# Kernel optimization log

Hardware: AMD Instinct MI355X
Metric: run time of the kernel (lower is better)

Reference implementation:

```python
import jax, jax.numpy as jnp
import numpy as np


def setup_inputs() -> dict:
    key = jax.random.key(0)
    k1, k2, k3 = jax.random.split(key, 3)
    B, S_TOT, HD = 2, 4096, 1024
    return {
        "q": jax.random.normal(k1, (B, S_TOT, HD), dtype=jnp.float32),
        "k": jax.random.normal(k2, (B, S_TOT, HD), dtype=jnp.float32),
        "v": jax.random.normal(k3, (B, S_TOT, HD), dtype=jnp.float32),
        "num_heads": 16,
        "num_shots": 4,
        "per_g": 64,
    }


def reference(q, k, v, num_heads, num_shots, per_g):
    # Equal-length shots: shot_latent_indices = [0, L, 2L, ..., s_tot] per batch.
    b, s_tot, hd = q.shape
    d = hd // num_heads
    L = s_tot // num_shots  # local shot length
    scale = 1.0 / jnp.sqrt(jnp.asarray(d, q.dtype))

    # [b, S, L, H, D]
    qs = q.reshape(b, num_shots, L, num_heads, d)
    ks = k.reshape(b, num_shots, L, num_heads, d)
    vs = v.reshape(b, num_shots, L, num_heads, d)

    # Global pool: first per_g tokens of each shot ('firstk'), shared by all shots.
    kg = ks[:, :, :per_g].reshape(b, num_shots * per_g, num_heads, d)  # [b, G, H, D]
    vg = vs[:, :, :per_g].reshape(b, num_shots * per_g, num_heads, d)

    # Block-local scores [b,S,H,L,L] and shared-global scores [b,S,H,L,G]
    s_loc = jnp.einsum("bsqhd,bskhd->bshqk", qs, ks) * scale
    s_glb = jnp.einsum("bsqhd,bghd->bshqg", qs, kg) * scale
    logits = jnp.concatenate([s_loc, s_glb], axis=-1)  # [b,S,H,L,L+G]
    p = jax.nn.softmax(logits, axis=-1)

    o_loc = jnp.einsum("bshqk,bskhd->bsqhd", p[..., :L], vs)
    o_glb = jnp.einsum("bshqg,bghd->bsqhd", p[..., L:], vg)
    out = (o_loc + o_glb).reshape(b, s_tot, hd)
    return out
```

## Files before the change

### kernel.cpp

```cpp
#include <hip/hip_runtime.h>
#include <hip/hip_bf16.h>

#define S_TOT 4096
#define HDIM  1024
#define NH    16
#define DH    64
#define L_    1024
#define NT    19

using bf16x8 = __attribute__((ext_vector_type(8))) short;
using f32x16 = __attribute__((ext_vector_type(16))) float;
using i32x4  = __attribute__((ext_vector_type(4))) int;

typedef const __attribute__((address_space(1))) unsigned int* gp1_t;
typedef __attribute__((address_space(3))) unsigned int* lp3_t;

__device__ __forceinline__ short f2bf(float f) {
    union { float f; unsigned u; } x; x.f = f;
    unsigned r = x.u + 0x7FFFu + ((x.u >> 16) & 1u);
    return (short)(r >> 16);
}

__device__ __forceinline__ unsigned cvt_pk_bf16(float lo, float hi) {
    unsigned r;
    asm("v_cvt_pk_bf16_f32 %0, %1, %2" : "=v"(r) : "v"(lo), "v"(hi));
    return r;
}

__device__ __forceinline__ float exp2_fast(float x) {
#if __has_builtin(__builtin_amdgcn_exp2f)
    return __builtin_amdgcn_exp2f(x);
#else
    return exp2f(x);
#endif
}

__device__ __forceinline__ void gload16(const void* g, void* l) {
    __builtin_amdgcn_global_load_lds((gp1_t)g, (lp3_t)(unsigned long)(l), 16, 0, 0);
}

__global__ __launch_bounds__(256) void prep_kv(
    const float* __restrict__ kf, const float* __restrict__ vf,
    short* __restrict__ kb, short* __restrict__ vb)
{
    __shared__ short st[64 * 70];
    const int bid = blockIdx.x, tid = threadIdx.x;
    if (bid < 1024) {
        const int gid = bid * 256 + tid;
        #pragma unroll
        for (int it = 0; it < 2; ++it) {
            size_t e = ((size_t)gid + (size_t)it * 262144) * 16;
            #pragma unroll
            for (int half = 0; half < 2; ++half) {
                float4 a = *(const float4*)(kf + e + half * 8);
                float4 c = *(const float4*)(kf + e + half * 8 + 4);
                bf16x8 r;
                r[0]=f2bf(a.x); r[1]=f2bf(a.y); r[2]=f2bf(a.z); r[3]=f2bf(a.w);
                r[4]=f2bf(c.x); r[5]=f2bf(c.y); r[6]=f2bf(c.z); r[7]=f2bf(c.w);
                *(bf16x8*)(kb + e + half * 8) = r;
            }
        }
    } else {
        const int vbid = bid - 1024;
        const int stile = vbid & 63, ht = (vbid >> 6) & 15, b = vbid >> 10;
        const int rt = tid >> 2, q4 = tid & 3;
        const float* src = vf + ((size_t)(b * S_TOT + stile * 64 + rt)) * HDIM + ht * 64 + q4 * 16;
        short* dst = st + rt * 70 + q4 * 16;
        #pragma unroll
        for (int i = 0; i < 4; ++i) {
            float4 x = *(const float4*)(src + i * 4);
            dst[i*4+0] = f2bf(x.x); dst[i*4+1] = f2bf(x.y);
            dst[i*4+2] = f2bf(x.z); dst[i*4+3] = f2bf(x.w);
        }
        __syncthreads();
        const int orow = tid >> 2, oq = tid & 3;
        bf16x8 o0, o1;
        #pragma unroll
        for (int j = 0; j < 8; ++j) o0[j] = st[(oq * 16 + j) * 70 + orow];
        #pragma unroll
        for (int j = 0; j < 8; ++j) o1[j] = st[(oq * 16 + 8 + j) * 70 + orow];
        short* dst2 = vb + ((size_t)((b * NH + ht) * 64 + orow)) * S_TOT + stile * 64 + oq * 16;
        *(bf16x8*)dst2 = o0;
        *(bf16x8*)(dst2 + 8) = o1;
    }
}

__global__ __launch_bounds__(256, 2) void attn_kernel(
    const float* __restrict__ qf, const short* __restrict__ kb,
    const short* __restrict__ vb, float* __restrict__ out)
{
    __shared__ __align__(16) char smem[32768];
    const int tid  = threadIdx.x;
    const int wave = tid >> 6, lane = tid & 63;
    const int hi   = lane >> 5, q32 = lane & 31;

    const int bidhw = blockIdx.x;
    const int bid = ((bidhw & 7) << 6) | (bidhw >> 3);
    const int qt = bid & 3, h = (bid >> 2) & 15, s = (bid >> 6) & 3, b = bid >> 8;

    const float CSC = 0.125f * 1.4426950408889634f;
    bf16x8 qv[2][4];
    #pragma unroll
    for (int qs = 0; qs < 2; ++qs) {
        const float* qp = qf + ((size_t)(b*S_TOT + s*L_ + qt*256 + wave*64 + qs*32 + q32)) * HDIM
                             + h * DH + hi * 8;
        #pragma unroll
        for (int d = 0; d < 4; ++d) {
            float4 x0 = *(const float4*)(qp + d * 16);
            float4 x1 = *(const float4*)(qp + d * 16 + 4);
            i32x4 u;
            u[0] = (int)cvt_pk_bf16(x0.x * CSC, x0.y * CSC);
            u[1] = (int)cvt_pk_bf16(x0.z * CSC, x0.w * CSC);
            u[2] = (int)cvt_pk_bf16(x1.x * CSC, x1.y * CSC);
            u[3] = (int)cvt_pk_bf16(x1.z * CSC, x1.w * CSC);
            qv[qs][d] = __builtin_bit_cast(bf16x8, u);
        }
    }

    const int cid = tid, row = cid >> 3;
    const int lch = (cid & 7) ^ (row & 7);
    const int krow = (row & 0x33) | ((row & 4) << 1) | ((row & 8) >> 1);
    const size_t ko = (size_t)krow * 2048 + (lch << 4);
    const size_t vo = (size_t)row  * 8192 + (lch << 4);
    const char* kbase = (const char*)kb + ((size_t)b * S_TOT) * 2048 + h * 128;
    const char* vbase = (const char*)vb + ((size_t)(b * NH + h)) * (64ull * 8192);

    auto abs_tile_of = [&](int t) -> int {
        if (t < 16) return s * 16 + t;
        int g = t - 16; if (g >= s) ++g;
        return g * 16;
    };
    auto stage = [&](int t, int bo) {
        const int at = abs_tile_of(t);
        const char* kp = kbase + (size_t)at * 131072;
        const char* vp = vbase + (size_t)at * 128;
        char* dst = smem + bo + wave * 1024;
        gload16(kp + ko,          dst);
        gload16(kp + ko + 65536,  dst + 4096);
        gload16(vp + vo,          dst + 8192);
        gload16(vp + vo + 262144, dst + 12288);
    };

    int qc[4];
    #pragma unroll
    for (int i = 0; i < 4; ++i)
        qc[i] = q32 * 128 + (((i * 2 + hi) ^ (q32 & 7)) << 4);

    f32x16 zro;
    #pragma unroll
    for (int r = 0; r < 16; ++r) zro[r] = 0.f;
    f32x16 acc[2][2];
    acc[0][0] = zro; acc[0][1] = zro; acc[1][0] = zro; acc[1][1] = zro;
    float ps[2] = {0.f, 0.f};

    stage(0, 0);
    int bufo = 0;
    for (int t = 0; t < NT; ++t) {
        if (t + 1 < NT) {
            stage(t + 1, bufo ^ 16384);
            asm volatile("s_waitcnt vmcnt(4)" ::: "memory");
        } else {
            asm volatile("s_waitcnt vmcnt(0)" ::: "memory");
        }
        __builtin_amdgcn_sched_barrier(0);
        __builtin_amdgcn_s_barrier();
        __builtin_amdgcn_sched_barrier(0);
        const char* sb = smem + bufo;

        #pragma unroll
        for (int half = 0; half < 2; ++half) {
            const int koff = half * 4096;
            f32x16 S[2];
            __builtin_amdgcn_s_setprio(1);
            bf16x8 f0 = *(const bf16x8*)(sb + koff + qc[0]);
            bf16x8 f1 = *(const bf16x8*)(sb + koff + qc[1]);
            bf16x8 f2 = *(const bf16x8*)(sb + koff + qc[2]);
            bf16x8 f3 = *(const bf16x8*)(sb + koff + qc[3]);
            #pragma unroll
            for (int qs = 0; qs < 2; ++qs) {
                f32x16 a = __builtin_amdgcn_mfma_f32_32x32x16_bf16(f0, qv[qs][0], zro, 0,0,0);
                a = __builtin_amdgcn_mfma_f32_32x32x16_bf16(f1, qv[qs][1], a, 0,0,0);
                a = __builtin_amdgcn_mfma_f32_32x32x16_bf16(f2, qv[qs][2], a, 0,0,0);
                a = __builtin_amdgcn_mfma_f32_32x32x16_bf16(f3, qv[qs][3], a, 0,0,0);
                S[qs] = a;
            }
            __builtin_amdgcn_s_setprio(0);

            if (t == 0) {
                #pragma unroll
                for (int qs = 0; qs < 2; ++qs)
                    #pragma unroll
                    for (int r = 0; r < 16; ++r)
                        S[qs][r] = exp2_fast(S[qs][r] + 1.0f);
            } else {
                #pragma unroll
                for (int qs = 0; qs < 2; ++qs)
                    #pragma unroll
                    for (int r = 0; r < 16; ++r)
                        S[qs][r] = exp2_fast(S[qs][r]);
            }
            #pragma unroll
            for (int qs = 0; qs < 2; ++qs) {
                float s0 = (S[qs][0] + S[qs][1]) + (S[qs][2] + S[qs][3]);
                float s1 = (S[qs][4] + S[qs][5]) + (S[qs][6] + S[qs][7]);
                float s2 = (S[qs][8] + S[qs][9]) + (S[qs][10] + S[qs][11]);
                float s3 = (S[qs][12] + S[qs][13]) + (S[qs][14] + S[qs][15]);
                ps[qs] += (s0 + s1) + (s2 + s3);
            }

            bf16x8 pf[2][2];
            #pragma unroll
            for (int qs = 0; qs < 2; ++qs) {
                i32x4 u;
                u[0] = (int)cvt_pk_bf16(S[qs][0],  S[qs][1]);
                u[1] = (int)cvt_pk_bf16(S[qs][2],  S[qs][3]);
                u[2] = (int)cvt_pk_bf16(S[qs][4],  S[qs][5]);
                u[3] = (int)cvt_pk_bf16(S[qs][6],  S[qs][7]);
                pf[qs][0] = __builtin_bit_cast(bf16x8, u);
                u[0] = (int)cvt_pk_bf16(S[qs][8],  S[qs][9]);
                u[1] = (int)cvt_pk_bf16(S[qs][10], S[qs][11]);
                u[2] = (int)cvt_pk_bf16(S[qs][12], S[qs][13]);
                u[3] = (int)cvt_pk_bf16(S[qs][14], S[qs][15]);
                pf[qs][1] = __builtin_bit_cast(bf16x8, u);
            }

            __builtin_amdgcn_s_setprio(1);
            bf16x8 w00 = *(const bf16x8*)(sb + 8192  + qc[2*half]);
            bf16x8 w01 = *(const bf16x8*)(sb + 8192  + qc[2*half+1]);
            bf16x8 w10 = *(const bf16x8*)(sb + 12288 + qc[2*half]);
            bf16x8 w11 = *(const bf16x8*)(sb + 12288 + qc[2*half+1]);
            #pragma unroll
            for (int qs = 0; qs < 2; ++qs) {
                acc[qs][0] = __builtin_amdgcn_mfma_f32_32x32x16_bf16(w00, pf[qs][0], acc[qs][0], 0,0,0);
                acc[qs][0] = __builtin_amdgcn_mfma_f32_32x32x16_bf16(w01, pf[qs][1], acc[qs][0], 0,0,0);
                acc[qs][1] = __builtin_amdgcn_mfma_f32_32x32x16_bf16(w10, pf[qs][0], acc[qs][1], 0,0,0);
                acc[qs][1] = __builtin_amdgcn_mfma_f32_32x32x16_bf16(w11, pf[qs][1], acc[qs][1], 0,0,0);
            }
            __builtin_amdgcn_s_setprio(0);
        }

        __builtin_amdgcn_sched_barrier(0);
        __builtin_amdgcn_s_barrier();
        __builtin_amdgcn_sched_barrier(0);
        bufo ^= 16384;
    }

    #pragma unroll
    for (int qs = 0; qs < 2; ++qs) {
        float tot = ps[qs] + __shfl_xor(ps[qs], 32);
        float inv = 1.0f / tot;
        const size_t orow = (size_t)(b*S_TOT + s*L_ + qt*256 + wave*64 + qs*32 + q32);
        float* op = out + orow * HDIM + h * DH;
        #pragma unroll
        for (int m = 0; m < 4; ++m) {
            float4 w0, w1;
            w0.x = acc[qs][0][4*m+0]*inv; w0.y = acc[qs][0][4*m+1]*inv;
            w0.z = acc[qs][0][4*m+2]*inv; w0.w = acc[qs][0][4*m+3]*inv;
            *(float4*)(op + 8*m + 4*hi) = w0;
            w1.x = acc[qs][1][4*m+0]*inv; w1.y = acc[qs][1][4*m+1]*inv;
            w1.z = acc[qs][1][4*m+2]*inv; w1.w = acc[qs][1][4*m+3]*inv;
            *(float4*)(op + 32 + 8*m + 4*hi) = w1;
        }
    }
}

extern "C" void kernel_launch(void* const* d_in, const int* in_sizes, int n_in,
                              void* d_out, int out_size, void* d_ws, size_t ws_size,
                              hipStream_t stream) {
    const float* q = (const float*)d_in[0];
    const float* k = (const float*)d_in[1];
    const float* v = (const float*)d_in[2];
    char* ws = (char*)d_ws;
    short* kbuf = (short*)(ws);
    short* vbuf = (short*)(ws + (16u << 20));
    prep_kv<<<dim3(3072), dim3(256), 0, stream>>>(k, v, kbuf, vbuf);
    attn_kernel<<<dim3(512), dim3(256), 0, stream>>>(q, kbuf, vbuf, (float*)d_out);
}
```

Baseline: 71.22 us.

## Deepen K/V prefetch to two-tile stages with quad LDS buffering

Doubles shared memory to 64KB so that two K/V tiles are loaded per stage and two stages are in flight. Each barrier pair now covers two tiles, which halves the number of barriers per tile and hides more global-load latency behind the MFMA work. In exchange, LDS per block doubles, which could limit blocks per CU. The prologue also adds a full vmcnt(0) drain, and the last stage loads tile 18 twice because of index clamping.

```diff
diff --git a/kernel.cpp b/kernel.cpp
--- a/kernel.cpp
+++ b/kernel.cpp
@@ -89,7 +89,7 @@
     const float* __restrict__ qf, const short* __restrict__ kb,
     const short* __restrict__ vb, float* __restrict__ out)
 {
-    __shared__ __align__(16) char smem[32768];
+    __shared__ __align__(16) char smem[65536];
     const int tid  = threadIdx.x;
     const int wave = tid >> 6, lane = tid & 63;
     const int hi   = lane >> 5, q32 = lane & 31;
@@ -130,11 +130,11 @@
         int g = t - 16; if (g >= s) ++g;
         return g * 16;
     };
-    auto stage = [&](int t, int bo) {
+    auto stage = [&](int t, int rbase) {
         const int at = abs_tile_of(t);
         const char* kp = kbase + (size_t)at * 131072;
         const char* vp = vbase + (size_t)at * 128;
-        char* dst = smem + bo + wave * 1024;
+        char* dst = smem + rbase + wave * 1024;
         gload16(kp + ko,          dst);
         gload16(kp + ko + 65536,  dst + 4096);
         gload16(vp + vo,          dst + 8192);
@@ -153,97 +153,105 @@
     acc[0][0] = zro; acc[0][1] = zro; acc[1][0] = zro; acc[1][1] = zro;
     float ps[2] = {0.f, 0.f};
 
+    #define CHUNK(RB, HF, W2) do {                                                 \
+        f32x16 S_[2];                                                              \
+        {                                                                          \
+            __builtin_amdgcn_s_setprio(1);                                         \
+            bf16x8 f0 = *(const bf16x8*)(smem + (RB) + (HF)*4096 + qc[0]);         \
+            bf16x8 f1 = *(const bf16x8*)(smem + (RB) + (HF)*4096 + qc[1]);         \
+            bf16x8 f2 = *(const bf16x8*)(smem + (RB) + (HF)*4096 + qc[2]);         \
+            bf16x8 f3 = *(const bf16x8*)(smem + (RB) + (HF)*4096 + qc[3]);         \
+            _Pragma("unroll")                                                      \
+            for (int qs = 0; qs < 2; ++qs) {                                       \
+                f32x16 a = __builtin_amdgcn_mfma_f32_32x32x16_bf16(f0, qv[qs][0], zro, 0,0,0); \
+                a = __builtin_amdgcn_mfma_f32_32x32x16_bf16(f1, qv[qs][1], a, 0,0,0); \
+                a = __builtin_amdgcn_mfma_f32_32x32x16_bf16(f2, qv[qs][2], a, 0,0,0); \
+                a = __builtin_amdgcn_mfma_f32_32x32x16_bf16(f3, qv[qs][3], a, 0,0,0); \
+                S_[qs] = a;                                                        \
+            }                                                                      \
+            __builtin_amdgcn_s_setprio(0);                                         \
+        }                                                                          \
+        _Pragma("unroll")                                                          \
+        for (int qs = 0; qs < 2; ++qs) {                                           \
+            _Pragma("unroll")                                                      \
+            for (int r = 0; r < 16; ++r)                                           \
+                S_[qs][r] = (W2) ? exp2_fast(S_[qs][r] + 1.0f)                     \
+                                 : exp2_fast(S_[qs][r]);                           \
+            float s0 = (S_[qs][0] + S_[qs][1]) + (S_[qs][2] + S_[qs][3]);          \
+            float s1 = (S_[qs][4] + S_[qs][5]) + (S_[qs][6] + S_[qs][7]);          \
+            float s2 = (S_[qs][8] + S_[qs][9]) + (S_[qs][10] + S_[qs][11]);        \
+            float s3 = (S_[qs][12] + S_[qs][13]) + (S_[qs][14] + S_[qs][15]);      \
+            ps[qs] += (s0 + s1) + (s2 + s3);                                       \
+        }                                                                          \
+        bf16x8 pf0_[2], pf1_[2];                                                   \
+        _Pragma("unroll")                                                          \
+        for (int qs = 0; qs < 2; ++qs) {                                           \
+            i32x4 u;                                                               \
+            u[0] = (int)cvt_pk_bf16(S_[qs][0],  S_[qs][1]);                        \
+            u[1] = (int)cvt_pk_bf16(S_[qs][2],  S_[qs][3]);                        \
+            u[2] = (int)cvt_pk_bf16(S_[qs][4],  S_[qs][5]);                        \
+            u[3] = (int)cvt_pk_bf16(S_[qs][6],  S_[qs][7]);                        \
+            pf0_[qs] = __builtin_bit_cast(bf16x8, u);                              \
+            u[0] = (int)cvt_pk_bf16(S_[qs][8],  S_[qs][9]);                        \
+            u[1] = (int)cvt_pk_bf16(S_[qs][10], S_[qs][11]);                       \
+            u[2] = (int)cvt_pk_bf16(S_[qs][12], S_[qs][13]);                       \
+            u[3] = (int)cvt_pk_bf16(S_[qs][14], S_[qs][15]);                       \
+            pf1_[qs] = __builtin_bit_cast(bf16x8, u);                              \
+        }                                                                          \
+        {                                                                          \
+            __builtin_amdgcn_s_setprio(1);                                         \
+            bf16x8 w00 = *(const bf16x8*)(smem + (RB) + 8192  + qc[2*(HF)]);       \
+            bf16x8 w01 = *(const bf16x8*)(smem + (RB) + 8192  + qc[2*(HF)+1]);     \
+            bf16x8 w10 = *(const bf16x8*)(smem + (RB) + 12288 + qc[2*(HF)]);       \
+            bf16x8 w11 = *(const bf16x8*)(smem + (RB) + 12288 + qc[2*(HF)+1]);     \
+            _Pragma("unroll")                                                      \
+            for (int qs = 0; qs < 2; ++qs) {                                       \
+                acc[qs][0] = __builtin_amdgcn_mfma_f32_32x32x16_bf16(w00, pf0_[qs], acc[qs][0], 0,0,0); \
+                acc[qs][0] = __builtin_amdgcn_mfma_f32_32x32x16_bf16(w01, pf1_[qs], acc[qs][0], 0,0,0); \
+                acc[qs][1] = __builtin_amdgcn_mfma_f32_32x32x16_bf16(w10, pf0_[qs], acc[qs][1], 0,0,0); \
+                acc[qs][1] = __builtin_amdgcn_mfma_f32_32x32x16_bf16(w11, pf1_[qs], acc[qs][1], 0,0,0); \
+            }                                                                      \
+            __builtin_amdgcn_s_setprio(0);                                         \
+        }                                                                          \
+    } while (0)
+
+    #define BARRIER() do {                                                         \
+        __builtin_amdgcn_sched_barrier(0);                                         \
+        __builtin_amdgcn_s_barrier();                                              \
+        __builtin_amdgcn_sched_barrier(0);                                         \
+    } while (0)
+
     stage(0, 0);
-    int bufo = 0;
-    for (int t = 0; t < NT; ++t) {
-        if (t + 1 < NT) {
-            stage(t + 1, bufo ^ 16384);
-            asm volatile("s_waitcnt vmcnt(4)" ::: "memory");
-        } else {
-            asm volatile("s_waitcnt vmcnt(0)" ::: "memory");
-        }
-        __builtin_amdgcn_sched_barrier(0);
-        __builtin_amdgcn_s_barrier();
-        __builtin_amdgcn_sched_barrier(0);
-        const char* sb = smem + bufo;
-
-        #pragma unroll
-        for (int half = 0; half < 2; ++half) {
-            const int koff = half * 4096;
-            f32x16 S[2];
-            __builtin_amdgcn_s_setprio(1);
-            bf16x8 f0 = *(const bf16x8*)(sb + koff + qc[0]);
-            bf16x8 f1 = *(const bf16x8*)(sb + koff + qc[1]);
-            bf16x8 f2 = *(const bf16x8*)(sb + koff + qc[2]);
-            bf16x8 f3 = *(const bf16x8*)(sb + koff + qc[3]);
-            #pragma unroll
-            for (int qs = 0; qs < 2; ++qs) {
-                f32x16 a = __builtin_amdgcn_mfma_f32_32x32x16_bf16(f0, qv[qs][0], zro, 0,0,0);
-                a = __builtin_amdgcn_mfma_f32_32x32x16_bf16(f1, qv[qs][1], a, 0,0,0);
-                a = __builtin_amdgcn_mfma_f32_32x32x16_bf16(f2, qv[qs][2], a, 0,0,0);
-                a = __builtin_amdgcn_mfma_f32_32x32x16_bf16(f3, qv[qs][3], a, 0,0,0);
-                S[qs] = a;
-            }
-            __builtin_amdgcn_s_setprio(0);
-
-            if (t == 0) {
-                #pragma unroll
-                for (int qs = 0; qs < 2; ++qs)
-                    #pragma unroll
-                    for (int r = 0; r < 16; ++r)
-                        S[qs][r] = exp2_fast(S[qs][r] + 1.0f);
-            } else {
-                #pragma unroll
-                for (int qs = 0; qs < 2; ++qs)
-                    #pragma unroll
-                    for (int r = 0; r < 16; ++r)
-                        S[qs][r] = exp2_fast(S[qs][r]);
-            }
-            #pragma unroll
-            for (int qs = 0; qs < 2; ++qs) {
-                float s0 = (S[qs][0] + S[qs][1]) + (S[qs][2] + S[qs][3]);
-                float s1 = (S[qs][4] + S[qs][5]) + (S[qs][6] + S[qs][7]);
-                float s2 = (S[qs][8] + S[qs][9]) + (S[qs][10] + S[qs][11]);
-                float s3 = (S[qs][12] + S[qs][13]) + (S[qs][14] + S[qs][15]);
-                ps[qs] += (s0 + s1) + (s2 + s3);
-            }
-
-            bf16x8 pf[2][2];
-            #pragma unroll
-            for (int qs = 0; qs < 2; ++qs) {
-                i32x4 u;
-                u[0] = (int)cvt_pk_bf16(S[qs][0],  S[qs][1]);
-                u[1] = (int)cvt_pk_bf16(S[qs][2],  S[qs][3]);
-                u[2] = (int)cvt_pk_bf16(S[qs][4],  S[qs][5]);
-                u[3] = (int)cvt_pk_bf16(S[qs][6],  S[qs][7]);
-                pf[qs][0] = __builtin_bit_cast(bf16x8, u);
-                u[0] = (int)cvt_pk_bf16(S[qs][8],  S[qs][9]);
-                u[1] = (int)cvt_pk_bf16(S[qs][10], S[qs][11]);
-                u[2] = (int)cvt_pk_bf16(S[qs][12], S[qs][13]);
-                u[3] = (int)cvt_pk_bf16(S[qs][14], S[qs][15]);
-                pf[qs][1] = __builtin_bit_cast(bf16x8, u);
-            }
-
-            __builtin_amdgcn_s_setprio(1);
-            bf16x8 w00 = *(const bf16x8*)(sb + 8192  + qc[2*half]);
-            bf16x8 w01 = *(const bf16x8*)(sb + 8192  + qc[2*half+1]);
-            bf16x8 w10 = *(const bf16x8*)(sb + 12288 + qc[2*half]);
-            bf16x8 w11 = *(const bf16x8*)(sb + 12288 + qc[2*half+1]);
-            #pragma unroll
-            for (int qs = 0; qs < 2; ++qs) {
-                acc[qs][0] = __builtin_amdgcn_mfma_f32_32x32x16_bf16(w00, pf[qs][0], acc[qs][0], 0,0,0);
-                acc[qs][0] = __builtin_amdgcn_mfma_f32_32x32x16_bf16(w01, pf[qs][1], acc[qs][0], 0,0,0);
-                acc[qs][1] = __builtin_amdgcn_mfma_f32_32x32x16_bf16(w10, pf[qs][0], acc[qs][1], 0,0,0);
-                acc[qs][1] = __builtin_amdgcn_mfma_f32_32x32x16_bf16(w11, pf[qs][1], acc[qs][1], 0,0,0);
-            }
-            __builtin_amdgcn_s_setprio(0);
-        }
-
-        __builtin_amdgcn_sched_barrier(0);
-        __builtin_amdgcn_s_barrier();
-        __builtin_amdgcn_sched_barrier(0);
-        bufo ^= 16384;
-    }
+    stage(1, 16384);
+    asm volatile("s_waitcnt vmcnt(0)" ::: "memory");
+    BARRIER();
+
+    stage(2, 32768);
+    stage(3, 49152);
+    asm volatile("s_waitcnt vmcnt(8)" ::: "memory");
+    BARRIER();
+    CHUNK(0, 0, 1); CHUNK(0, 1, 1);
+    CHUNK(16384, 0, 0); CHUNK(16384, 1, 0);
+    BARRIER();
+
+    for (int j = 1; j < 9; ++j) {
+        const int rS = (j & 1) ? 0 : 32768;
+        const int rC = (j & 1) ? 32768 : 0;
+        int ts0 = 2*j + 2, ts1 = 2*j + 3;
+        if (ts0 > 18) ts0 = 18;
+        if (ts1 > 18) ts1 = 18;
+        stage(ts0, rS);
+        stage(ts1, rS + 16384);
+        asm volatile("s_waitcnt vmcnt(8)" ::: "memory");
+        BARRIER();
+        CHUNK(rC, 0, 0); CHUNK(rC, 1, 0);
+        CHUNK(rC + 16384, 0, 0); CHUNK(rC + 16384, 1, 0);
+        BARRIER();
+    }
+
+    asm volatile("s_waitcnt vmcnt(0)" ::: "memory");
+    BARRIER();
+    CHUNK(32768, 0, 0); CHUNK(32768, 1, 0);
 
     #pragma unroll
     for (int qs = 0; qs < 2; ++qs) {
```

Measured after the change: 75.27 us. 5.7% more time.

## Use 8 waves with one query block each and triple-buffered K/V staging

Applied to the files above, without the earlier changes.

Blocks grow from 256 to 512 threads, and each wave now owns 32 query rows instead of 64, which halves accumulator registers per wave. Staging moves from double to triple buffering in 48KB of LDS, prefetching two tiles ahead with a single barrier per iteration. The single-tile-half loop is replaced by interleaved score MFMAs over the full 64-key tile. The aim is more waves in flight and deeper latency hiding. The cost is more LDS per block, which may limit occupancy, and each K/V fragment read from LDS is reused by fewer MFMAs.

```diff
diff --git a/kernel.cpp b/kernel.cpp
--- a/kernel.cpp
+++ b/kernel.cpp
@@ -85,11 +85,11 @@
     }
 }
 
-__global__ __launch_bounds__(256, 2) void attn_kernel(
+__global__ __launch_bounds__(512, 2) void attn_kernel(
     const float* __restrict__ qf, const short* __restrict__ kb,
     const short* __restrict__ vb, float* __restrict__ out)
 {
-    __shared__ __align__(16) char smem[32768];
+    __shared__ __align__(16) char smem[49152];
     const int tid  = threadIdx.x;
     const int wave = tid >> 6, lane = tid & 63;
     const int hi   = lane >> 5, q32 = lane & 31;
@@ -99,25 +99,23 @@
     const int qt = bid & 3, h = (bid >> 2) & 15, s = (bid >> 6) & 3, b = bid >> 8;
 
     const float CSC = 0.125f * 1.4426950408889634f;
-    bf16x8 qv[2][4];
-    #pragma unroll
-    for (int qs = 0; qs < 2; ++qs) {
-        const float* qp = qf + ((size_t)(b*S_TOT + s*L_ + qt*256 + wave*64 + qs*32 + q32)) * HDIM
-                             + h * DH + hi * 8;
-        #pragma unroll
-        for (int d = 0; d < 4; ++d) {
-            float4 x0 = *(const float4*)(qp + d * 16);
-            float4 x1 = *(const float4*)(qp + d * 16 + 4);
-            i32x4 u;
-            u[0] = (int)cvt_pk_bf16(x0.x * CSC, x0.y * CSC);
-            u[1] = (int)cvt_pk_bf16(x0.z * CSC, x0.w * CSC);
-            u[2] = (int)cvt_pk_bf16(x1.x * CSC, x1.y * CSC);
-            u[3] = (int)cvt_pk_bf16(x1.z * CSC, x1.w * CSC);
-            qv[qs][d] = __builtin_bit_cast(bf16x8, u);
-        }
-    }
-
-    const int cid = tid, row = cid >> 3;
+    const float* qp = qf + ((size_t)(b*S_TOT + s*L_ + qt*256 + wave*32 + q32)) * HDIM
+                         + h * DH + hi * 8;
+    bf16x8 qv[4];
+    #pragma unroll
+    for (int d = 0; d < 4; ++d) {
+        float4 x0 = *(const float4*)(qp + d * 16);
+        float4 x1 = *(const float4*)(qp + d * 16 + 4);
+        i32x4 u;
+        u[0] = (int)cvt_pk_bf16(x0.x * CSC, x0.y * CSC);
+        u[1] = (int)cvt_pk_bf16(x0.z * CSC, x0.w * CSC);
+        u[2] = (int)cvt_pk_bf16(x1.x * CSC, x1.y * CSC);
+        u[3] = (int)cvt_pk_bf16(x1.z * CSC, x1.w * CSC);
+        qv[d] = __builtin_bit_cast(bf16x8, u);
+    }
+
+    const int cid = wave * 64 + lane;
+    const int row = cid >> 3;
     const int lch = (cid & 7) ^ (row & 7);
     const int krow = (row & 0x33) | ((row & 4) << 1) | ((row & 8) >> 1);
     const size_t ko = (size_t)krow * 2048 + (lch << 4);
@@ -134,11 +132,9 @@
         const int at = abs_tile_of(t);
         const char* kp = kbase + (size_t)at * 131072;
         const char* vp = vbase + (size_t)at * 128;
-        char* dst = smem + bo + wave * 1024;
-        gload16(kp + ko,          dst);
-        gload16(kp + ko + 65536,  dst + 4096);
-        gload16(vp + vo,          dst + 8192);
-        gload16(vp + vo + 262144, dst + 12288);
+        char* dK = smem + bo + wave * 1024;
+        gload16(kp + ko, dK);
+        gload16(vp + vo, dK + 8192);
     };
 
     int qc[4];
@@ -149,118 +145,109 @@
     f32x16 zro;
     #pragma unroll
     for (int r = 0; r < 16; ++r) zro[r] = 0.f;
-    f32x16 acc[2][2];
-    acc[0][0] = zro; acc[0][1] = zro; acc[1][0] = zro; acc[1][1] = zro;
-    float ps[2] = {0.f, 0.f};
+    f32x16 acc0 = zro, acc1 = zro;
+    float ps = 0.f;
 
     stage(0, 0);
-    int bufo = 0;
+    stage(1, 16384);
+    asm volatile("s_waitcnt vmcnt(0)" ::: "memory");
+
+    int rd = 0, nx = 16384, st = 32768;
     for (int t = 0; t < NT; ++t) {
-        if (t + 1 < NT) {
-            stage(t + 1, bufo ^ 16384);
-            asm volatile("s_waitcnt vmcnt(4)" ::: "memory");
-        } else {
-            asm volatile("s_waitcnt vmcnt(0)" ::: "memory");
-        }
         __builtin_amdgcn_sched_barrier(0);
         __builtin_amdgcn_s_barrier();
         __builtin_amdgcn_sched_barrier(0);
-        const char* sb = smem + bufo;
-
-        #pragma unroll
-        for (int half = 0; half < 2; ++half) {
-            const int koff = half * 4096;
-            f32x16 S[2];
+
+        if (t + 2 < NT) stage(t + 2, st);
+
+        const float bias = (t == 0) ? 1.0f : 0.0f;
+        const char* sb = smem + rd;
+
+        f32x16 sA, sB;
+        {
             __builtin_amdgcn_s_setprio(1);
-            bf16x8 f0 = *(const bf16x8*)(sb + koff + qc[0]);
-            bf16x8 f1 = *(const bf16x8*)(sb + koff + qc[1]);
-            bf16x8 f2 = *(const bf16x8*)(sb + koff + qc[2]);
-            bf16x8 f3 = *(const bf16x8*)(sb + koff + qc[3]);
-            #pragma unroll
-            for (int qs = 0; qs < 2; ++qs) {
-                f32x16 a = __builtin_amdgcn_mfma_f32_32x32x16_bf16(f0, qv[qs][0], zro, 0,0,0);
-                a = __builtin_amdgcn_mfma_f32_32x32x16_bf16(f1, qv[qs][1], a, 0,0,0);
-                a = __builtin_amdgcn_mfma_f32_32x32x16_bf16(f2, qv[qs][2], a, 0,0,0);
-                a = __builtin_amdgcn_mfma_f32_32x32x16_bf16(f3, qv[qs][3], a, 0,0,0);
-                S[qs] = a;
-            }
+            bf16x8 a0 = *(const bf16x8*)(sb + qc[0]);
+            bf16x8 b0 = *(const bf16x8*)(sb + 4096 + qc[0]);
+            sA = __builtin_amdgcn_mfma_f32_32x32x16_bf16(a0, qv[0], zro, 0,0,0);
+            sB = __builtin_amdgcn_mfma_f32_32x32x16_bf16(b0, qv[0], zro, 0,0,0);
+            bf16x8 a1 = *(const bf16x8*)(sb + qc[1]);
+            bf16x8 b1 = *(const bf16x8*)(sb + 4096 + qc[1]);
+            sA = __builtin_amdgcn_mfma_f32_32x32x16_bf16(a1, qv[1], sA, 0,0,0);
+            sB = __builtin_amdgcn_mfma_f32_32x32x16_bf16(b1, qv[1], sB, 0,0,0);
+            bf16x8 a2 = *(const bf16x8*)(sb + qc[2]);
+            bf16x8 b2 = *(const bf16x8*)(sb + 4096 + qc[2]);
+            sA = __builtin_amdgcn_mfma_f32_32x32x16_bf16(a2, qv[2], sA, 0,0,0);
+            sB = __builtin_amdgcn_mfma_f32_32x32x16_bf16(b2, qv[2], sB, 0,0,0);
+            bf16x8 a3 = *(const bf16x8*)(sb + qc[3]);
+            bf16x8 b3 = *(const bf16x8*)(sb + 4096 + qc[3]);
+            sA = __builtin_amdgcn_mfma_f32_32x32x16_bf16(a3, qv[3], sA, 0,0,0);
+            sB = __builtin_amdgcn_mfma_f32_32x32x16_bf16(b3, qv[3], sB, 0,0,0);
             __builtin_amdgcn_s_setprio(0);
-
-            if (t == 0) {
-                #pragma unroll
-                for (int qs = 0; qs < 2; ++qs)
-                    #pragma unroll
-                    for (int r = 0; r < 16; ++r)
-                        S[qs][r] = exp2_fast(S[qs][r] + 1.0f);
-            } else {
-                #pragma unroll
-                for (int qs = 0; qs < 2; ++qs)
-                    #pragma unroll
-                    for (int r = 0; r < 16; ++r)
-                        S[qs][r] = exp2_fast(S[qs][r]);
-            }
-            #pragma unroll
-            for (int qs = 0; qs < 2; ++qs) {
-                float s0 = (S[qs][0] + S[qs][1]) + (S[qs][2] + S[qs][3]);
-                float s1 = (S[qs][4] + S[qs][5]) + (S[qs][6] + S[qs][7]);
-                float s2 = (S[qs][8] + S[qs][9]) + (S[qs][10] + S[qs][11]);
-                float s3 = (S[qs][12] + S[qs][13]) + (S[qs][14] + S[qs][15]);
-                ps[qs] += (s0 + s1) + (s2 + s3);
-            }
-
-            bf16x8 pf[2][2];
-            #pragma unroll
-            for (int qs = 0; qs < 2; ++qs) {
-                i32x4 u;
-                u[0] = (int)cvt_pk_bf16(S[qs][0],  S[qs][1]);
-                u[1] = (int)cvt_pk_bf16(S[qs][2],  S[qs][3]);
-                u[2] = (int)cvt_pk_bf16(S[qs][4],  S[qs][5]);
-                u[3] = (int)cvt_pk_bf16(S[qs][6],  S[qs][7]);
-                pf[qs][0] = __builtin_bit_cast(bf16x8, u);
-                u[0] = (int)cvt_pk_bf16(S[qs][8],  S[qs][9]);
-                u[1] = (int)cvt_pk_bf16(S[qs][10], S[qs][11]);
-                u[2] = (int)cvt_pk_bf16(S[qs][12], S[qs][13]);
-                u[3] = (int)cvt_pk_bf16(S[qs][14], S[qs][15]);
-                pf[qs][1] = __builtin_bit_cast(bf16x8, u);
-            }
-
+        }
+
+        #pragma unroll
+        for (int r = 0; r < 16; ++r) { float p = exp2_fast(sA[r] + bias); sA[r] = p; ps += p; }
+        #pragma unroll
+        for (int r = 0; r < 16; ++r) { float p = exp2_fast(sB[r] + bias); sB[r] = p; ps += p; }
+
+        bf16x8 pf0, pf1, pf2, pf3;
+        {
+            i32x4 u;
+            u[0]=(int)cvt_pk_bf16(sA[0],sA[1]);  u[1]=(int)cvt_pk_bf16(sA[2],sA[3]);
+            u[2]=(int)cvt_pk_bf16(sA[4],sA[5]);  u[3]=(int)cvt_pk_bf16(sA[6],sA[7]);
+            pf0 = __builtin_bit_cast(bf16x8, u);
+            u[0]=(int)cvt_pk_bf16(sA[8],sA[9]);  u[1]=(int)cvt_pk_bf16(sA[10],sA[11]);
+            u[2]=(int)cvt_pk_bf16(sA[12],sA[13]);u[3]=(int)cvt_pk_bf16(sA[14],sA[15]);
+            pf1 = __builtin_bit_cast(bf16x8, u);
+            u[0]=(int)cvt_pk_bf16(sB[0],sB[1]);  u[1]=(int)cvt_pk_bf16(sB[2],sB[3]);
+            u[2]=(int)cvt_pk_bf16(sB[4],sB[5]);  u[3]=(int)cvt_pk_bf16(sB[6],sB[7]);
+            pf2 = __builtin_bit_cast(bf16x8, u);
+            u[0]=(int)cvt_pk_bf16(sB[8],sB[9]);  u[1]=(int)cvt_pk_bf16(sB[10],sB[11]);
+            u[2]=(int)cvt_pk_bf16(sB[12],sB[13]);u[3]=(int)cvt_pk_bf16(sB[14],sB[15]);
+            pf3 = __builtin_bit_cast(bf16x8, u);
+        }
+
+        {
             __builtin_amdgcn_s_setprio(1);
-            bf16x8 w00 = *(const bf16x8*)(sb + 8192  + qc[2*half]);
-            bf16x8 w01 = *(const bf16x8*)(sb + 8192  + qc[2*half+1]);
-            bf16x8 w10 = *(const bf16x8*)(sb + 12288 + qc[2*half]);
-            bf16x8 w11 = *(const bf16x8*)(sb + 12288 + qc[2*half+1]);
-            #pragma unroll
-            for (int qs = 0; qs < 2; ++qs) {
-                acc[qs][0] = __builtin_amdgcn_mfma_f32_32x32x16_bf16(w00, pf[qs][0], acc[qs][0], 0,0,0);
-                acc[qs][0] = __builtin_amdgcn_mfma_f32_32x32x16_bf16(w01, pf[qs][1], acc[qs][0], 0,0,0);
-                acc[qs][1] = __builtin_amdgcn_mfma_f32_32x32x16_bf16(w10, pf[qs][0], acc[qs][1], 0,0,0);
-                acc[qs][1] = __builtin_amdgcn_mfma_f32_32x32x16_bf16(w11, pf[qs][1], acc[qs][1], 0,0,0);
-            }
+            bf16x8 v00 = *(const bf16x8*)(sb + 8192  + qc[0]);
+            bf16x8 v10 = *(const bf16x8*)(sb + 12288 + qc[0]);
+            acc0 = __builtin_amdgcn_mfma_f32_32x32x16_bf16(v00, pf0, acc0, 0,0,0);
+            acc1 = __builtin_amdgcn_mfma_f32_32x32x16_bf16(v10, pf0, acc1, 0,0,0);
+            bf16x8 v01 = *(const bf16x8*)(sb + 8192  + qc[1]);
+            bf16x8 v11 = *(const bf16x8*)(sb + 12288 + qc[1]);
+            acc0 = __builtin_amdgcn_mfma_f32_32x32x16_bf16(v01, pf1, acc0, 0,0,0);
+            acc1 = __builtin_amdgcn_mfma_f32_32x32x16_bf16(v11, pf1, acc1, 0,0,0);
+            bf16x8 v02 = *(const bf16x8*)(sb + 8192  + qc[2]);
+            bf16x8 v12 = *(const bf16x8*)(sb + 12288 + qc[2]);
+            acc0 = __builtin_amdgcn_mfma_f32_32x32x16_bf16(v02, pf2, acc0, 0,0,0);
+            acc1 = __builtin_amdgcn_mfma_f32_32x32x16_bf16(v12, pf2, acc1, 0,0,0);
+            bf16x8 v03 = *(const bf16x8*)(sb + 8192  + qc[3]);
+            bf16x8 v13 = *(const bf16x8*)(sb + 12288 + qc[3]);
+            acc0 = __builtin_amdgcn_mfma_f32_32x32x16_bf16(v03, pf3, acc0, 0,0,0);
+            acc1 = __builtin_amdgcn_mfma_f32_32x32x16_bf16(v13, pf3, acc1, 0,0,0);
             __builtin_amdgcn_s_setprio(0);
         }
 
-        __builtin_amdgcn_sched_barrier(0);
-        __builtin_amdgcn_s_barrier();
-        __builtin_amdgcn_sched_barrier(0);
-        bufo ^= 16384;
-    }
-
-    #pragma unroll
-    for (int qs = 0; qs < 2; ++qs) {
-        float tot = ps[qs] + __shfl_xor(ps[qs], 32);
-        float inv = 1.0f / tot;
-        const size_t orow = (size_t)(b*S_TOT + s*L_ + qt*256 + wave*64 + qs*32 + q32);
-        float* op = out + orow * HDIM + h * DH;
-        #pragma unroll
-        for (int m = 0; m < 4; ++m) {
-            float4 w0, w1;
-            w0.x = acc[qs][0][4*m+0]*inv; w0.y = acc[qs][0][4*m+1]*inv;
-            w0.z = acc[qs][0][4*m+2]*inv; w0.w = acc[qs][0][4*m+3]*inv;
-            *(float4*)(op + 8*m + 4*hi) = w0;
-            w1.x = acc[qs][1][4*m+0]*inv; w1.y = acc[qs][1][4*m+1]*inv;
-            w1.z = acc[qs][1][4*m+2]*inv; w1.w = acc[qs][1][4*m+3]*inv;
-            *(float4*)(op + 32 + 8*m + 4*hi) = w1;
-        }
+        if (t + 1 < NT) {
+            if (t + 2 < NT) { asm volatile("s_waitcnt vmcnt(2)" ::: "memory"); }
+            else            { asm volatile("s_waitcnt vmcnt(0)" ::: "memory"); }
+        }
+        int tmp = rd; rd = nx; nx = st; st = tmp;
+    }
+
+    float tot = ps + __shfl_xor(ps, 32);
+    float inv = 1.0f / tot;
+    const size_t orow = (size_t)(b*S_TOT + s*L_ + qt*256 + wave*32 + q32);
+    float* op = out + orow * HDIM + h * DH;
+    #pragma unroll
+    for (int m = 0; m < 4; ++m) {
+        float4 w0, w1;
+        w0.x = acc0[4*m+0]*inv; w0.y = acc0[4*m+1]*inv;
+        w0.z = acc0[4*m+2]*inv; w0.w = acc0[4*m+3]*inv;
+        *(float4*)(op + 8*m + 4*hi) = w0;
+        w1.x = acc1[4*m+0]*inv; w1.y = acc1[4*m+1]*inv;
+        w1.z = acc1[4*m+2]*inv; w1.w = acc1[4*m+3]*inv;
+        *(float4*)(op + 32 + 8*m + 4*hi) = w1;
     }
 }
 
@@ -274,5 +261,5 @@
     short* kbuf = (short*)(ws);
     short* vbuf = (short*)(ws + (16u << 20));
     prep_kv<<<dim3(3072), dim3(256), 0, stream>>>(k, v, kbuf, vbuf);
-    attn_kernel<<<dim3(512), dim3(256), 0, stream>>>(q, kbuf, vbuf, (float*)d_out);
-}
+    attn_kernel<<<dim3(512), dim3(512), 0, stream>>>(q, kbuf, vbuf, (float*)d_out);
+}
```

Measured after the change: 73.27 us. +2.9%, slower.
